# Kernel optimization log

Measured on AMD Instinct MI355X. Metric: run time of the kernel, lower is better.

## Reference

```python
import jax, jax.numpy as jnp
import numpy as np

# Ordered bi-bi mechanism, species order per _build_species_list:
# [E, EA, EQ, EAB, A, B, P, Q] -> indices 0..7
# Transitions: E+A<->EA, EA+B<->EAB, EAB<->EQ+P, EQ<->E+Q (all reversible)
N_SPECIES = 8
N_TRANS = 4

# forward: rate * [enzyme] * prod([substrates]); -1 = no factor (padded)
ENZ_F = np.array([0, 1, 3, 2], dtype=np.int32)          # E, EA, EAB, EQ
SUB_F = np.array([[4], [5], [-1], [-1]], dtype=np.int32)  # A, B, -, -
# reverse: rate * [to-enzyme] * prod([products])
ENZ_R = np.array([1, 3, 2, 0], dtype=np.int32)          # EA, EAB, EQ, E
PROD_R = np.array([[-1], [-1], [6], [7]], dtype=np.int32)  # -, -, P, Q
REV_MASK = np.array([1.0, 1.0, 1.0, 1.0], dtype=np.float32)

# Stoichiometry (n_trans, n_species), applied as dydt += v_net[:,None]*S[i]
S_FORWARD = np.array([
    [-1,  1,  0,  0, -1,  0,  0,  0],
    [ 0, -1,  0,  1,  0, -1,  0,  0],
    [ 0,  0,  1, -1,  0,  0,  1,  0],
    [ 1,  0, -1,  0,  0,  0,  0,  1],
], dtype=np.float32)


def _masked_gather_prod(y, idx):
    # y: (B, n_species); idx: (n_trans, k) with -1 padding
    safe = jnp.maximum(idx, 0)
    g = y[:, safe.reshape(-1)].reshape(y.shape[0], idx.shape[0], idx.shape[1])  # (B,T,k)
    g = jnp.where(idx[None, :, :] >= 0, g, 1.0)
    return jnp.prod(g, axis=-1)  # (B, T)


def setup_inputs() -> dict:
    key = jax.random.key(0)
    k1, k2, k3 = jax.random.split(key, 3)
    B = 2_000_000
    return {
        "t": jnp.zeros((1,), dtype=jnp.float32),
        "y": jax.random.uniform(k1, (B, N_SPECIES), dtype=jnp.float32),
        "forward_rates": jax.random.uniform(k2, (B, N_TRANS), dtype=jnp.float32),
        "reverse_rates": jax.random.uniform(k3, (B, N_TRANS), dtype=jnp.float32),
    }


def reference(t, y, forward_rates, reverse_rates):
    enz_f = jnp.asarray(ENZ_F)
    enz_r = jnp.asarray(ENZ_R)
    sub_f = jnp.asarray(SUB_F)
    prod_r = jnp.asarray(PROD_R)
    S = jnp.asarray(S_FORWARD)
    rev_mask = jnp.asarray(REV_MASK)

    # v_forward[b,i] = k_f[b,i] * y[b, enz_f[i]] * prod_j y[b, sub_f[i,j]]
    v_f = forward_rates * y[:, enz_f] * _masked_gather_prod(y, sub_f)
    # v_reverse analogous, zeroed for irreversible transitions
    v_r = reverse_rates * y[:, enz_r] * _masked_gather_prod(y, prod_r) * rev_mask[None, :]
    v_net = v_f - v_r  # (B, T)
    # dydt[b,s] = sum_i v_net[b,i] * S[i,s]
    return jnp.einsum("bt,ts->bs", v_net, S)
```

## Files before the change

### kernel.cpp

```cpp
#include <hip/hip_runtime.h>


typedef float v4f __attribute__((ext_vector_type(4)));

#define ITERS 4

__global__ __launch_bounds__(256) void ode_kernel(
    const float4* __restrict__ y4,
    const float4* __restrict__ kf4,
    const float4* __restrict__ kr4,
    float4* __restrict__ out4,
    int n2)
{
    const int stride = gridDim.x * blockDim.x;
    const int t0 = blockIdx.x * blockDim.x + threadIdx.x;
    const int h = t0 & 1;

    const float4* __restrict__ rp = h ? kr4 : kf4;

    int   t[ITERS];
    bool  vld[ITERS];
    float4 q[ITERS], mine[ITERS];

    #pragma unroll
    for (int k = 0; k < ITERS; ++k) {
        t[k]   = t0 + k * stride;
        vld[k] = t[k] < n2;
        if (vld[k]) {
            q[k]    = y4[t[k]];
            mine[k] = rp[t[k] >> 1];
        }
    }

    #pragma unroll
    for (int k = 0; k < ITERS; ++k) {
        if (!vld[k]) continue;

        float4 qq = q[k];
        float4 p;
        p.x = __shfl_xor(qq.x, 1);
        p.y = __shfl_xor(qq.y, 1);
        p.z = __shfl_xor(qq.z, 1);
        p.w = __shfl_xor(qq.w, 1);

        float4 ya = h ? p  : qq;
        float4 yb = h ? qq : p;

        float4 mm = mine[k];
        float4 other;
        other.x = __shfl_xor(mm.x, 1);
        other.y = __shfl_xor(mm.y, 1);
        other.z = __shfl_xor(mm.z, 1);
        other.w = __shfl_xor(mm.w, 1);

        float4 f = h ? other : mm;
        float4 r = h ? mm : other;

        float E  = ya.x, EA = ya.y, EQ = ya.z, EAB = ya.w;
        float A  = yb.x, Bc = yb.y, P  = yb.z, Q   = yb.w;

        float v0 = f.x * E   * A  - r.x * EA;
        float v1 = f.y * EA  * Bc - r.y * EAB;
        float v2 = f.z * EAB      - r.z * EQ * P;
        float v3 = f.w * EQ       - r.w * E  * Q;

        float4 o;
        if (h == 0) {
            o.x = v3 - v0;
            o.y = v0 - v1;
            o.z = v2 - v3;
            o.w = v1 - v2;
        } else {
            o.x = -v0;
            o.y = -v1;
            o.z =  v2;
            o.w =  v3;
        }

        v4f ov;
        ov.x = o.x; ov.y = o.y; ov.z = o.z; ov.w = o.w;
        __builtin_nontemporal_store(ov, (v4f*)(out4 + t[k]));
    }
}

extern "C" void kernel_launch(void* const* d_in, const int* in_sizes, int n_in,
                              void* d_out, int out_size, void* d_ws, size_t ws_size,
                              hipStream_t stream) {
    const float4* y4  = (const float4*)d_in[1];
    const float4* kf4 = (const float4*)d_in[2];
    const float4* kr4 = (const float4*)d_in[3];
    float4* out4 = (float4*)d_out;
    int B  = in_sizes[1] / 8;
    int n2 = 2 * B;

    int block = 256;
    int grid  = (n2 + block * ITERS - 1) / (block * ITERS);
    ode_kernel<<<grid, block, 0, stream>>>(y4, kf4, kr4, out4, n2);
}
```

Measured before the change: 173.6 us.

## Process one element per thread without lane shuffles, using nontemporal loads

Replaces the two-threads-per-element scheme, which exchanged halves via shuffles, with one thread per batch element. Each thread loads both halves of y and its forward and reverse rates directly, using nontemporal loads. A fast path without bounds checks is added for full iterations, and the per-thread unroll drops from four to two. This removes the shuffle and select overhead, but each load instruction now touches strided addresses for y and out.

```diff
diff --git a/kernel.cpp b/kernel.cpp
--- a/kernel.cpp
+++ b/kernel.cpp
@@ -3,97 +3,87 @@
 
 typedef float v4f __attribute__((ext_vector_type(4)));
 
-#define ITERS 4
+#define ITERS 2
+
+__device__ __forceinline__ void ode_elem(v4f ya, v4f yb, v4f f, v4f r,
+                                         v4f& oa, v4f& ob) {
+    float E  = ya.x, EA = ya.y, EQ = ya.z, EAB = ya.w;
+    float A  = yb.x, Bc = yb.y, P  = yb.z, Q   = yb.w;
+
+    float v0 = f.x * E   * A  - r.x * EA;
+    float v1 = f.y * EA  * Bc - r.y * EAB;
+    float v2 = f.z * EAB      - r.z * EQ * P;
+    float v3 = f.w * EQ       - r.w * E  * Q;
+
+    oa.x = v3 - v0;
+    oa.y = v0 - v1;
+    oa.z = v2 - v3;
+    oa.w = v1 - v2;
+    ob.x = -v0;
+    ob.y = -v1;
+    ob.z =  v2;
+    ob.w =  v3;
+}
 
 __global__ __launch_bounds__(256) void ode_kernel(
-    const float4* __restrict__ y4,
-    const float4* __restrict__ kf4,
-    const float4* __restrict__ kr4,
-    float4* __restrict__ out4,
-    int n2)
+    const v4f* __restrict__ y4,
+    const v4f* __restrict__ kf4,
+    const v4f* __restrict__ kr4,
+    v4f* __restrict__ out4,
+    int B)
 {
     const int stride = gridDim.x * blockDim.x;
-    const int t0 = blockIdx.x * blockDim.x + threadIdx.x;
-    const int h = t0 & 1;
+    const int e0 = blockIdx.x * blockDim.x + threadIdx.x;
 
-    const float4* __restrict__ rp = h ? kr4 : kf4;
-
-    int   t[ITERS];
-    bool  vld[ITERS];
-    float4 q[ITERS], mine[ITERS];
-
-    #pragma unroll
-    for (int k = 0; k < ITERS; ++k) {
-        t[k]   = t0 + k * stride;
-        vld[k] = t[k] < n2;
-        if (vld[k]) {
-            q[k]    = y4[t[k]];
-            mine[k] = rp[t[k] >> 1];
-        }
-    }
-
-    #pragma unroll
-    for (int k = 0; k < ITERS; ++k) {
-        if (!vld[k]) continue;
-
-        float4 qq = q[k];
-        float4 p;
-        p.x = __shfl_xor(qq.x, 1);
-        p.y = __shfl_xor(qq.y, 1);
-        p.z = __shfl_xor(qq.z, 1);
-        p.w = __shfl_xor(qq.w, 1);
-
-        float4 ya = h ? p  : qq;
-        float4 yb = h ? qq : p;
-
-        float4 mm = mine[k];
-        float4 other;
-        other.x = __shfl_xor(mm.x, 1);
-        other.y = __shfl_xor(mm.y, 1);
-        other.z = __shfl_xor(mm.z, 1);
-        other.w = __shfl_xor(mm.w, 1);
-
-        float4 f = h ? other : mm;
-        float4 r = h ? mm : other;
-
-        float E  = ya.x, EA = ya.y, EQ = ya.z, EAB = ya.w;
-        float A  = yb.x, Bc = yb.y, P  = yb.z, Q   = yb.w;
-
-        float v0 = f.x * E   * A  - r.x * EA;
-        float v1 = f.y * EA  * Bc - r.y * EAB;
-        float v2 = f.z * EAB      - r.z * EQ * P;
-        float v3 = f.w * EQ       - r.w * E  * Q;
-
-        float4 o;
-        if (h == 0) {
-            o.x = v3 - v0;
-            o.y = v0 - v1;
-            o.z = v2 - v3;
-            o.w = v1 - v2;
-        } else {
-            o.x = -v0;
-            o.y = -v1;
-            o.z =  v2;
-            o.w =  v3;
+    if (e0 + (ITERS - 1) * stride < B) {
+        v4f ya[ITERS], yb[ITERS], f[ITERS], r[ITERS];
+        #pragma unroll
+        for (int k = 0; k < ITERS; ++k) {
+            int e = e0 + k * stride;
+            ya[k] = __builtin_nontemporal_load(y4 + 2 * e);
+            yb[k] = __builtin_nontemporal_load(y4 + 2 * e + 1);
+            f[k]  = __builtin_nontemporal_load(kf4 + e);
+            r[k]  = __builtin_nontemporal_load(kr4 + e);
         }
 
-        v4f ov;
-        ov.x = o.x; ov.y = o.y; ov.z = o.z; ov.w = o.w;
-        __builtin_nontemporal_store(ov, (v4f*)(out4 + t[k]));
+        v4f oa[ITERS], ob[ITERS];
+        #pragma unroll
+        for (int k = 0; k < ITERS; ++k)
+            ode_elem(ya[k], yb[k], f[k], r[k], oa[k], ob[k]);
+
+        #pragma unroll
+        for (int k = 0; k < ITERS; ++k) {
+            int e = e0 + k * stride;
+            __builtin_nontemporal_store(oa[k], out4 + 2 * e);
+            __builtin_nontemporal_store(ob[k], out4 + 2 * e + 1);
+        }
+    } else {
+        for (int k = 0; k < ITERS; ++k) {
+            int e = e0 + k * stride;
+            if (e < B) {
+                v4f ya = __builtin_nontemporal_load(y4 + 2 * e);
+                v4f yb = __builtin_nontemporal_load(y4 + 2 * e + 1);
+                v4f f  = __builtin_nontemporal_load(kf4 + e);
+                v4f r  = __builtin_nontemporal_load(kr4 + e);
+                v4f oa, ob;
+                ode_elem(ya, yb, f, r, oa, ob);
+                __builtin_nontemporal_store(oa, out4 + 2 * e);
+                __builtin_nontemporal_store(ob, out4 + 2 * e + 1);
+            }
+        }
     }
 }
 
 extern "C" void kernel_launch(void* const* d_in, const int* in_sizes, int n_in,
                               void* d_out, int out_size, void* d_ws, size_t ws_size,
                               hipStream_t stream) {
-    const float4* y4  = (const float4*)d_in[1];
-    const float4* kf4 = (const float4*)d_in[2];
-    const float4* kr4 = (const float4*)d_in[3];
-    float4* out4 = (float4*)d_out;
-    int B  = in_sizes[1] / 8;
-    int n2 = 2 * B;
+    const v4f* y4  = (const v4f*)d_in[1];
+    const v4f* kf4 = (const v4f*)d_in[2];
+    const v4f* kr4 = (const v4f*)d_in[3];
+    v4f* out4 = (v4f*)d_out;
+    int B = in_sizes[1] / 8;
 
     int block = 256;
-    int grid  = (n2 + block * ITERS - 1) / (block * ITERS);
-    ode_kernel<<<grid, block, 0, stream>>>(y4, kf4, kr4, out4, n2);
+    int grid  = (B + block * ITERS - 1) / (block * ITERS);
+    ode_kernel<<<grid, block, 0, stream>>>(y4, kf4, kr4, out4, B);
 }
```

Result: faster. 168.3 us (-3.0%).
